# Performance work log

Hardware: AMD Instinct MI355X
Metric: run time of the kernel (lower is better)

Reference implementation:

```python
import jax, jax.numpy as jnp
import numpy as np

N_NODES = 100000
N_EDGES = 1600000
D_IN = 64
D_OUT = 64
BN_EPS = 1e-5


def setup_inputs() -> dict:
    key = jax.random.key(0)
    k_x, k_src, k_dst, k_ew, k_w = jax.random.split(key, 5)
    x = jax.random.normal(k_x, (N_NODES, D_IN), dtype=jnp.float32)
    edge_src = jax.random.randint(k_src, (N_EDGES,), 0, N_NODES, dtype=jnp.int32)
    edge_dst = jax.random.randint(k_dst, (N_EDGES,), 0, N_NODES, dtype=jnp.int32)
    edge_weight = jax.random.uniform(k_ew, (N_EDGES,), dtype=jnp.float32)
    # Xavier-uniform weight, zero bias (reset_parameters)
    limit = float(np.sqrt(6.0 / (D_IN + D_OUT)))
    W = jax.random.uniform(k_w, (D_IN, D_OUT), dtype=jnp.float32, minval=-limit, maxval=limit)
    bias = jnp.zeros((D_OUT,), dtype=jnp.float32)
    gamma = jnp.ones((D_OUT,), dtype=jnp.float32)
    beta = jnp.zeros((D_OUT,), dtype=jnp.float32)
    return {"x": x, "edge_src": edge_src, "edge_dst": edge_dst,
            "edge_weight": edge_weight, "W": W, "bias": bias,
            "gamma": gamma, "beta": beta}


def reference(x, edge_src, edge_dst, edge_weight, W, bias, gamma, beta):
    # GraphConvolution: support = x @ W  -> [N, D_OUT]
    support = jnp.matmul(x, W)
    # spmm(adj, support) with adj in COO form: out[d] += w_e * support[s]
    msgs = edge_weight[:, None] * support[edge_src]        # [E, D_OUT]
    agg = jax.ops.segment_sum(msgs, edge_dst, num_segments=N_NODES)
    out = agg + bias
    # BatchNorm1d (training mode: batch statistics over node dim)
    mean = jnp.mean(out, axis=0)
    var = jnp.var(out, axis=0)
    out = (out - mean) * jax.lax.rsqrt(var + BN_EPS) * gamma + beta
    # ReLU activation; dropout is identity in deterministic/inference mode
    return jax.nn.relu(out)
```

## Files before the change

kernel.cpp:

```cpp
#include <hip/hip_runtime.h>
#include <hip/hip_bf16.h>

#define NN 100000
#define NE 1600000
#define DD 64
#define NCOARSE 392
#define GEMM_TILES 1563
#define PLACE_EPB 2048
#define PLACE_BLOCKS 784
#define CAP 4736

__device__ inline unsigned short f2bf(float f) {
    __hip_bfloat16 h = __float2bfloat16(f);
    unsigned short s; __builtin_memcpy(&s, &h, 2); return s;
}

__global__ __launch_bounds__(512) void k_zero(int* __restrict__ gcnt) {
    if (threadIdx.x < NCOARSE) gcnt[threadIdx.x] = 0;
}

__global__ __launch_bounds__(256) void k_gemm_scatter(const float* __restrict__ x,
                                                      const float* __restrict__ Wg,
                                                      unsigned* __restrict__ support2,
                                                      const int* __restrict__ esrc,
                                                      const int* __restrict__ edst,
                                                      const float* __restrict__ ew,
                                                      int* __restrict__ gcnt,
                                                      int2* __restrict__ permA) {
    if (blockIdx.x < PLACE_BLOCKS) {
        const int blk = blockIdx.x;
        __shared__ int h[NCOARSE];
        __shared__ int loff[NCOARSE];
        for (int i = threadIdx.x; i < NCOARSE; i += 256) h[i] = 0;
        __syncthreads();
        const int e0 = blk * PLACE_EPB;
        int dreg[8];
#pragma unroll
        for (int k = 0; k < 8; ++k) {
            const int e = e0 + k * 256 + threadIdx.x;
            dreg[k] = (e < NE) ? edst[e] : -1;
            if (dreg[k] >= 0) atomicAdd(&h[dreg[k] >> 8], 1);
        }
        __syncthreads();
        for (int i = threadIdx.x; i < NCOARSE; i += 256) {
            const int hc = h[i];
            loff[i] = i * CAP + ((hc > 0) ? atomicAdd(&gcnt[i], hc) : 0);
        }
        __syncthreads();
#pragma unroll
        for (int k = 0; k < 8; ++k) {
            if (dreg[k] >= 0) {
                const int e = e0 + k * 256 + threadIdx.x;
                const int d = dreg[k];
                const int c = d >> 8;
                const int p = atomicAdd(&loff[c], 1);
                if (p < c * CAP + CAP)
                    permA[p] = make_int2(esrc[e] | ((d & 255) << 17), __float_as_int(ew[e]));
            }
        }
        return;
    }

    __shared__ float Xs[64 * DD];
    const int r0 = (blockIdx.x - PLACE_BLOCKS) * 64;
    const int nrows = (r0 + 64 <= NN) ? 64 : (NN - r0);
    const int t = threadIdx.x;

    const float4* xg = (const float4*)(x + (size_t)r0 * DD);
    for (int i = t; i < nrows * 16; i += 256) {
        const int row = i >> 4, k4 = i & 15;
        *(float4*)&Xs[row * 64 + ((k4 ^ (row & 15)) << 2)] = xg[i];
    }
    if (nrows < 64) {
        for (int i = nrows * 16 + t; i < 64 * 16; i += 256)
            ((float4*)Xs)[i] = make_float4(0.f, 0.f, 0.f, 0.f);
    }
    __syncthreads();

    const int lane = t & 63;
    const int w = __builtin_amdgcn_readfirstlane(t >> 6);
    const float* Wp = Wg + w * 16;

    float acc[16];
#pragma unroll
    for (int c = 0; c < 16; ++c) acc[c] = 0.f;

#pragma unroll 4
    for (int k4 = 0; k4 < 16; ++k4) {
        const float4 xv = *(const float4*)&Xs[lane * 64 + ((k4 ^ (lane & 15)) << 2)];
        const float* wr = Wp + k4 * 4 * DD;
#pragma unroll
        for (int c = 0; c < 16; ++c) {
            acc[c] = fmaf(xv.x, wr[c],          acc[c]);
            acc[c] = fmaf(xv.y, wr[DD + c],     acc[c]);
            acc[c] = fmaf(xv.z, wr[2 * DD + c], acc[c]);
            acc[c] = fmaf(xv.w, wr[3 * DD + c], acc[c]);
        }
    }

    __syncthreads();
    unsigned* Us = (unsigned*)Xs;
#pragma unroll
    for (int j = 0; j < 8; ++j) {
        const unsigned p = (unsigned)f2bf(acc[2 * j]) |
                           ((unsigned)f2bf(acc[2 * j + 1]) << 16);
        const int cp = 8 * w + j;
        Us[lane * 32 + ((cp + lane) & 31)] = p;
    }
    __syncthreads();
    uint4* sg = (uint4*)(support2 + (size_t)r0 * 32);
#pragma unroll
    for (int it = 0; it < 2; ++it) {
        const int g4 = t + it * 256;
        const int row = g4 >> 3, c0 = (g4 & 7) << 2;
        if (row < nrows) {
            uint4 v;
            v.x = Us[row * 32 + ((c0 + 0 + row) & 31)];
            v.y = Us[row * 32 + ((c0 + 1 + row) & 31)];
            v.z = Us[row * 32 + ((c0 + 2 + row) & 31)];
            v.w = Us[row * 32 + ((c0 + 3 + row) & 31)];
            sg[g4] = v;
        }
    }
}

__global__ __launch_bounds__(1024, 8) void k_sortgather(const int* __restrict__ gcnt,
                                                        const int2* __restrict__ permA,
                                                        const uint4* __restrict__ support4,
                                                        float* __restrict__ out,
                                                        float* __restrict__ pstat) {
    __shared__ int2 eL[CAP];
    __shared__ unsigned short idx16[CAP];
    __shared__ int cnt[256], st[257], cur[256], wtot[4];
    __shared__ float red[16][128];

    const int c = blockIdx.x, t = threadIdx.x;
    const int cs = c * CAP;
    const int sz = min(gcnt[c], CAP);
    const int wave = t >> 6, lane = t & 63;

    for (int j = t; j < sz; j += 1024) eL[j] = permA[cs + j];
    if (t < 256) cnt[t] = 0;
    __syncthreads();

    for (int j = t; j < sz; j += 1024)
        atomicAdd(&cnt[(eL[j].x >> 17) & 255], 1);
    __syncthreads();

    int v = 0, xv = 0;
    if (wave < 4) {
        v = cnt[t]; xv = v;
#pragma unroll
        for (int o = 1; o < 64; o <<= 1) {
            int u = __shfl_up(xv, o, 64);
            if (lane >= o) xv += u;
        }
        if (lane == 63) wtot[wave] = xv;
    }
    __syncthreads();
    if (t < 4) {
        int w0 = wtot[t], xw = w0;
#pragma unroll
        for (int o = 1; o < 4; o <<= 1) {
            int u = __shfl_up(xw, o, 64);
            if (t >= o) xw += u;
        }
        wtot[t] = xw - w0;
    }
    __syncthreads();
    if (wave < 4) {
        const int base = wtot[wave] + xv - v;
        st[t] = base;
        cur[t] = base;
    }
    if (t == 0) st[256] = sz;
    __syncthreads();

    for (int j = t; j < sz; j += 1024) {
        int p = atomicAdd(&cur[(eL[j].x >> 17) & 255], 1);
        idx16[p] = (unsigned short)j;
    }
    __syncthreads();

    const int sub = lane >> 3, q = lane & 7;
    const int node0 = c * 256;
    float sacc[8] = {0.f, 0.f, 0.f, 0.f, 0.f, 0.f, 0.f, 0.f};
    float sqacc[8] = {0.f, 0.f, 0.f, 0.f, 0.f, 0.f, 0.f, 0.f};
    for (int n = wave; n < 256; n += 16) {
        const int bs = st[n], be = st[n + 1];
        float acc[8] = {0.f, 0.f, 0.f, 0.f, 0.f, 0.f, 0.f, 0.f};
        for (int j0 = bs; j0 < be; j0 += 8) {
            const int j = j0 + sub;
            if (j < be) {
                const int2 m = eL[idx16[j]];
                const uint4 p = support4[(size_t)(m.x & 0x1FFFF) * 8 + q];
                const float w = __int_as_float(m.y);
                acc[0] = fmaf(w, __uint_as_float(p.x << 16), acc[0]);
                acc[1] = fmaf(w, __uint_as_float(p.x & 0xffff0000u), acc[1]);
                acc[2] = fmaf(w, __uint_as_float(p.y << 16), acc[2]);
                acc[3] = fmaf(w, __uint_as_float(p.y & 0xffff0000u), acc[3]);
                acc[4] = fmaf(w, __uint_as_float(p.z << 16), acc[4]);
                acc[5] = fmaf(w, __uint_as_float(p.z & 0xffff0000u), acc[5]);
                acc[6] = fmaf(w, __uint_as_float(p.w << 16), acc[6]);
                acc[7] = fmaf(w, __uint_as_float(p.w & 0xffff0000u), acc[7]);
            }
        }
#pragma unroll
        for (int i = 0; i < 8; ++i) {
            acc[i] += __shfl_xor(acc[i], 8, 64);
            acc[i] += __shfl_xor(acc[i], 16, 64);
            acc[i] += __shfl_xor(acc[i], 32, 64);
        }
        const int node = node0 + n;
        if (sub == 0 && node < NN) {
            float* op = out + (size_t)node * DD + q * 8;
            *(float4*)op = make_float4(acc[0], acc[1], acc[2], acc[3]);
            *(float4*)(op + 4) = make_float4(acc[4], acc[5], acc[6], acc[7]);
#pragma unroll
            for (int k = 0; k < 8; ++k) {
                sacc[k] += acc[k];
                sqacc[k] = fmaf(acc[k], acc[k], sqacc[k]);
            }
        }
    }

    if (sub == 0) {
#pragma unroll
        for (int k = 0; k < 8; ++k) {
            red[wave][q * 8 + k] = sacc[k];
            red[wave][64 + q * 8 + k] = sqacc[k];
        }
    }
    __syncthreads();
    if (t < 128) {
        float a = 0.f;
#pragma unroll
        for (int wv = 0; wv < 16; ++wv) a += red[wv][t];
        pstat[c * 128 + t] = a;
    }
}

__global__ __launch_bounds__(128) void k_finstats(const float* __restrict__ pstat,
                                                  float* __restrict__ ss,
                                                  const float* __restrict__ gamma,
                                                  const float* __restrict__ beta) {
    const int t = threadIdx.x;
    float acc = 0.f;
    for (int b = 0; b < NCOARSE; ++b)
        acc += pstat[b * 128 + t];
    __shared__ float red[2 * DD];
    red[t] = acc;
    __syncthreads();
    if (t < DD) {
        const float invn = 1.0f / NN;
        float mean = red[t] * invn;
        float var = fmaxf(red[DD + t] * invn - mean * mean, 0.f);
        float sc = rsqrtf(var + 1e-5f) * gamma[t];
        ss[t] = sc;
        ss[DD + t] = beta[t] - mean * sc;
    }
}

__global__ __launch_bounds__(256) void k_final(float* __restrict__ out,
                                               const float* __restrict__ ss) {
    const size_t idx = ((size_t)blockIdx.x * 256 + threadIdx.x) * 4;
    const int c = (int)(idx & 63);
    float4 v = *(const float4*)(out + idx);
    float4 o;
    o.x = fmaxf(fmaf(v.x, ss[c + 0], ss[DD + c + 0]), 0.f);
    o.y = fmaxf(fmaf(v.y, ss[c + 1], ss[DD + c + 1]), 0.f);
    o.z = fmaxf(fmaf(v.z, ss[c + 2], ss[DD + c + 2]), 0.f);
    o.w = fmaxf(fmaf(v.w, ss[c + 3], ss[DD + c + 3]), 0.f);
    *(float4*)(out + idx) = o;
}

extern "C" void kernel_launch(void* const* d_in, const int* in_sizes, int n_in,
                              void* d_out, int out_size, void* d_ws, size_t ws_size,
                              hipStream_t stream) {
    const float* x     = (const float*)d_in[0];
    const int*   esrc  = (const int*)d_in[1];
    const int*   edst  = (const int*)d_in[2];
    const float* ew    = (const float*)d_in[3];
    const float* W     = (const float*)d_in[4];
    const float* gamma = (const float*)d_in[6];
    const float* beta  = (const float*)d_in[7];
    float*       out   = (float*)d_out;

    char* ws = (char*)d_ws;
    unsigned* support2 = (unsigned*)ws;  ws += (size_t)NN * DD * 2;
    int2*     permA  = (int2*)ws;     ws += (size_t)NCOARSE * CAP * 8;
    int*   gcnt   = (int*)ws;    ws += NCOARSE * 4;
    float* ss     = (float*)ws;  ws += 128 * 4;
    float* pstat  = (float*)ws;  ws += (size_t)NCOARSE * 128 * 4;

    k_zero        <<<1, 512, 0, stream>>>(gcnt);
    k_gemm_scatter<<<PLACE_BLOCKS + GEMM_TILES, 256, 0, stream>>>(
                      x, W, support2, esrc, edst, ew, gcnt, permA);
    k_sortgather  <<<NCOARSE, 1024, 0, stream>>>(gcnt, permA,
                      (const uint4*)support2, out, pstat);
    k_finstats    <<<1, 128, 0, stream>>>(pstat, ss, gamma, beta);
    k_final       <<<NN * DD / 4 / 256, 256, 0, stream>>>(out, ss);
}
```

Before: 203.6 us.

## Fuse BN stats finalization into normalize kernel and double edges per placement block

Merges the single-block statistics finalizer and the elementwise BN+ReLU pass into one grid-stride kernel. Each of its 256 blocks redundantly reduces the per-chunk partial sums and keeps the scale/shift in shared memory, which removes one launch and the global ss round trip. Separately, the edge-placement phase now handles 4096 edges per block in half as many blocks, and it reloads edst in the second pass instead of holding it in registers. This trades register pressure and block count for repeated edst reads and fewer, longer placement blocks.

```diff
diff --git a/kernel.cpp b/kernel.cpp
--- a/kernel.cpp
+++ b/kernel.cpp
@@ -6,8 +6,8 @@
 #define DD 64
 #define NCOARSE 392
 #define GEMM_TILES 1563
-#define PLACE_EPB 2048
-#define PLACE_BLOCKS 784
+#define PLACE_EPB 4096
+#define PLACE_BLOCKS 392
 #define CAP 4736
 
 __device__ inline unsigned short f2bf(float f) {
@@ -34,12 +34,10 @@
         for (int i = threadIdx.x; i < NCOARSE; i += 256) h[i] = 0;
         __syncthreads();
         const int e0 = blk * PLACE_EPB;
-        int dreg[8];
-#pragma unroll
-        for (int k = 0; k < 8; ++k) {
+#pragma unroll 4
+        for (int k = 0; k < 16; ++k) {
             const int e = e0 + k * 256 + threadIdx.x;
-            dreg[k] = (e < NE) ? edst[e] : -1;
-            if (dreg[k] >= 0) atomicAdd(&h[dreg[k] >> 8], 1);
+            if (e < NE) atomicAdd(&h[edst[e] >> 8], 1);
         }
         __syncthreads();
         for (int i = threadIdx.x; i < NCOARSE; i += 256) {
@@ -47,11 +45,11 @@
             loff[i] = i * CAP + ((hc > 0) ? atomicAdd(&gcnt[i], hc) : 0);
         }
         __syncthreads();
-#pragma unroll
-        for (int k = 0; k < 8; ++k) {
-            if (dreg[k] >= 0) {
-                const int e = e0 + k * 256 + threadIdx.x;
-                const int d = dreg[k];
+#pragma unroll 4
+        for (int k = 0; k < 16; ++k) {
+            const int e = e0 + k * 256 + threadIdx.x;
+            if (e < NE) {
+                const int d = edst[e];
                 const int c = d >> 8;
                 const int p = atomicAdd(&loff[c], 1);
                 if (p < c * CAP + CAP)
@@ -240,38 +238,42 @@
     }
 }
 
-__global__ __launch_bounds__(128) void k_finstats(const float* __restrict__ pstat,
-                                                  float* __restrict__ ss,
-                                                  const float* __restrict__ gamma,
-                                                  const float* __restrict__ beta) {
+__global__ __launch_bounds__(256) void k_finalstats(const float* __restrict__ pstat,
+                                                    const float* __restrict__ gamma,
+                                                    const float* __restrict__ beta,
+                                                    float* __restrict__ out) {
+    __shared__ float red[128];
+    __shared__ float ssl[128];
     const int t = threadIdx.x;
-    float acc = 0.f;
-    for (int b = 0; b < NCOARSE; ++b)
-        acc += pstat[b * 128 + t];
-    __shared__ float red[2 * DD];
-    red[t] = acc;
+    if (t < 128) {
+        float acc = 0.f;
+        for (int b = 0; b < NCOARSE; ++b)
+            acc += pstat[b * 128 + t];
+        red[t] = acc;
+    }
     __syncthreads();
     if (t < DD) {
         const float invn = 1.0f / NN;
-        float mean = red[t] * invn;
-        float var = fmaxf(red[DD + t] * invn - mean * mean, 0.f);
-        float sc = rsqrtf(var + 1e-5f) * gamma[t];
-        ss[t] = sc;
-        ss[DD + t] = beta[t] - mean * sc;
-    }
-}
-
-__global__ __launch_bounds__(256) void k_final(float* __restrict__ out,
-                                               const float* __restrict__ ss) {
-    const size_t idx = ((size_t)blockIdx.x * 256 + threadIdx.x) * 4;
-    const int c = (int)(idx & 63);
-    float4 v = *(const float4*)(out + idx);
-    float4 o;
-    o.x = fmaxf(fmaf(v.x, ss[c + 0], ss[DD + c + 0]), 0.f);
-    o.y = fmaxf(fmaf(v.y, ss[c + 1], ss[DD + c + 1]), 0.f);
-    o.z = fmaxf(fmaf(v.z, ss[c + 2], ss[DD + c + 2]), 0.f);
-    o.w = fmaxf(fmaf(v.w, ss[c + 3], ss[DD + c + 3]), 0.f);
-    *(float4*)(out + idx) = o;
+        const float mean = red[t] * invn;
+        const float var = fmaxf(red[DD + t] * invn - mean * mean, 0.f);
+        const float sc = rsqrtf(var + 1e-5f) * gamma[t];
+        ssl[t] = sc;
+        ssl[DD + t] = beta[t] - mean * sc;
+    }
+    __syncthreads();
+
+    float4* out4 = (float4*)out;
+    const int total4 = NN * DD / 4;
+    for (int i = blockIdx.x * 256 + t; i < total4; i += 256 * 256) {
+        const int c = (i & 15) << 2;
+        float4 v = out4[i];
+        float4 o;
+        o.x = fmaxf(fmaf(v.x, ssl[c + 0], ssl[DD + c + 0]), 0.f);
+        o.y = fmaxf(fmaf(v.y, ssl[c + 1], ssl[DD + c + 1]), 0.f);
+        o.z = fmaxf(fmaf(v.z, ssl[c + 2], ssl[DD + c + 2]), 0.f);
+        o.w = fmaxf(fmaf(v.w, ssl[c + 3], ssl[DD + c + 3]), 0.f);
+        out4[i] = o;
+    }
 }
 
 extern "C" void kernel_launch(void* const* d_in, const int* in_sizes, int n_in,
@@ -290,7 +292,6 @@
     unsigned* support2 = (unsigned*)ws;  ws += (size_t)NN * DD * 2;
     int2*     permA  = (int2*)ws;     ws += (size_t)NCOARSE * CAP * 8;
     int*   gcnt   = (int*)ws;    ws += NCOARSE * 4;
-    float* ss     = (float*)ws;  ws += 128 * 4;
     float* pstat  = (float*)ws;  ws += (size_t)NCOARSE * 128 * 4;
 
     k_zero        <<<1, 512, 0, stream>>>(gcnt);
@@ -298,6 +299,5 @@
                       x, W, support2, esrc, edst, ew, gcnt, permA);
     k_sortgather  <<<NCOARSE, 1024, 0, stream>>>(gcnt, permA,
                       (const uint4*)support2, out, pstat);
-    k_finstats    <<<1, 128, 0, stream>>>(pstat, ss, gamma, beta);
-    k_final       <<<NN * DD / 4 / 256, 256, 0, stream>>>(out, ss);
-}
+    k_finalstats  <<<256, 256, 0, stream>>>(pstat, gamma, beta, out);
+}
```

After: 203.4 us. About the same (-0.1%).
